# Kernel tuning notes

Measured on AMD Instinct MI355X. Metric: run time of the kernel, lower is better.

Reference implementation:

```python
import jax, jax.numpy as jnp
import numpy as np

SPARSITY_RATIO = 0.1


def setup_inputs() -> dict:
    key = jax.random.key(0)
    x = jax.random.normal(key, (4, 4096, 2048), dtype=jnp.float32)
    return {"x": x}


def reference(x):
    # x: [batch, seq_len, n_embd]
    B, S, D = x.shape
    k = max(1, int(D * SPARSITY_RATIO))
    # top-k by absolute value along the feature dim
    _, topk_idx = jax.lax.top_k(jnp.abs(x), k)  # [B, S, k]
    # scatter 1.0 at top-k positions (matches torch scatter_ mask construction)
    b = jnp.arange(B)[:, None, None]
    s = jnp.arange(S)[None, :, None]
    mask = jnp.zeros_like(x).at[b, s, topk_idx].set(1.0)
    scale = jnp.asarray(D / k, dtype=x.dtype)
    return x * mask * scale
```

## Files before the change

kernel.cpp:

```cpp
#include <hip/hip_runtime.h>


constexpr int D_DIM = 2048;
constexpr int K_SEL = 204;
constexpr int NT    = 256;
constexpr int EPL   = 32;
constexpr int RPW   = 4;

__device__ __forceinline__ int dpp_reduce_add(int x) {
    x += __builtin_amdgcn_update_dpp(0, x, 0x111, 0xF, 0xF, true);
    x += __builtin_amdgcn_update_dpp(0, x, 0x112, 0xF, 0xF, true);
    x += __builtin_amdgcn_update_dpp(0, x, 0x114, 0xF, 0xF, true);
    x += __builtin_amdgcn_update_dpp(0, x, 0x118, 0xF, 0xF, true);
    x += __builtin_amdgcn_update_dpp(0, x, 0x142, 0xA, 0xF, false);
    x += __builtin_amdgcn_update_dpp(0, x, 0x143, 0xC, 0xF, false);
    return __builtin_amdgcn_readlane(x, 63);
}

__device__ __forceinline__ int count_ge(const unsigned (&a)[EPL], unsigned t) {
    int c0 = 0, c1 = 0, c2 = 0, c3 = 0;
#pragma unroll
    for (int j = 0; j < EPL; j += 4) {
        c0 += (a[j + 0] >= t) ? 1 : 0;
        c1 += (a[j + 1] >= t) ? 1 : 0;
        c2 += (a[j + 2] >= t) ? 1 : 0;
        c3 += (a[j + 3] >= t) ? 1 : 0;
    }
    return dpp_reduce_add((c0 + c1) + (c2 + c3));
}

__device__ __forceinline__ void finish_row(const unsigned (&a)[EPL], unsigned signs,
                                           bool exact, unsigned thr, unsigned T,
                                           float* __restrict__ outr, int lane) {
    const float scale = 2048.0f / 204.0f;
    float4* op = reinterpret_cast<float4*>(outr);

    if (!exact) {
        int ge_pack = 0;
#pragma unroll
        for (int j = 0; j < EPL; ++j) {
            ge_pack += (a[j] > T) ? 1 : 0;
            ge_pack += (a[j] == T) ? (1 << 16) : 0;
        }
        const int tot = dpp_reduce_add(ge_pack);
        const int cnt_gt = tot & 0xFFFF;
        const int neq = tot >> 16;
        const int r = K_SEL - cnt_gt;

        if (neq != r) {
            const unsigned long long lt =
                (lane == 0) ? 0ull : (~0ull >> (64 - lane));
            int base = 0;
            for (int b = 0; b < 8; ++b) {
                unsigned long long m[4];
#pragma unroll
                for (int e = 0; e < 4; ++e) m[e] = __ballot(a[4 * b + e] == T);
                int cm = 0;
#pragma unroll
                for (int e = 0; e < 4; ++e) cm += __popcll(m[e] & lt);
                int partial = 0;
                float v[4];
#pragma unroll
                for (int e = 0; e < 4; ++e) {
                    const int j = 4 * b + e;
                    const int rank = base + cm + partial;
                    const bool eq = (a[j] == T);
                    const bool sel = (a[j] > T) || (eq && rank < r);
                    const float val =
                        __uint_as_float(a[j] | (((signs >> j) & 1u) << 31)) * scale;
                    v[e] = sel ? val : 0.0f;
                    partial += (int)((m[e] >> lane) & 1ull);
                }
                op[b * 64 + lane] = make_float4(v[0], v[1], v[2], v[3]);
#pragma unroll
                for (int e = 0; e < 4; ++e) base += __popcll(m[e]);
            }
            return;
        }
        thr = T;
    }

#pragma unroll
    for (int b = 0; b < 8; ++b) {
        float v[4];
#pragma unroll
        for (int e = 0; e < 4; ++e) {
            const int j = 4 * b + e;
            const float val =
                __uint_as_float(a[j] | (((signs >> j) & 1u) << 31)) * scale;
            v[e] = (a[j] >= thr) ? val : 0.0f;
        }
        op[b * 64 + lane] = make_float4(v[0], v[1], v[2], v[3]);
    }
}

__global__ __launch_bounds__(NT) void sparse_topk_kernel(const float* __restrict__ x,
                                                         float* __restrict__ out) {
    const int wave = threadIdx.x >> 6;
    const int lane = threadIdx.x & 63;
    const long long wid = (long long)blockIdx.x * 4 + wave;
    const float* base = x + wid * RPW * D_DIM;
    float* obase = out + wid * RPW * D_DIM;

    float4 nf[8];
    {
        const float4* p = reinterpret_cast<const float4*>(base);
#pragma unroll
        for (int b = 0; b < 8; ++b) nf[b] = p[b * 64 + lane];
    }

#pragma unroll 1
    for (int r = 0; r < RPW; ++r) {
        unsigned a[EPL];
        unsigned signs = 0u;
#pragma unroll
        for (int b = 0; b < 8; ++b) {
            const unsigned w0 = __float_as_uint(nf[b].x);
            const unsigned w1 = __float_as_uint(nf[b].y);
            const unsigned w2 = __float_as_uint(nf[b].z);
            const unsigned w3 = __float_as_uint(nf[b].w);
            a[4 * b + 0] = w0 & 0x7fffffffu; signs |= (w0 >> 31) << (4 * b + 0);
            a[4 * b + 1] = w1 & 0x7fffffffu; signs |= (w1 >> 31) << (4 * b + 1);
            a[4 * b + 2] = w2 & 0x7fffffffu; signs |= (w2 >> 31) << (4 * b + 2);
            a[4 * b + 3] = w3 & 0x7fffffffu; signs |= (w3 >> 31) << (4 * b + 3);
        }

        if (r + 1 < RPW) {
            const float4* pn = reinterpret_cast<const float4*>(base + (r + 1) * D_DIM);
#pragma unroll
            for (int b = 0; b < 8; ++b) nf[b] = pn[b * 64 + lane];
        }

        unsigned lo = 0u, hi = 0x7F800000u;
        unsigned thr = 0u;
        bool exact = false;
        int step = 0, lastcnt = 0;
#pragma unroll 1
        while (hi - lo > 1u) {
            unsigned mid;
            if (step == 0)      mid = 0x3FD28F5Cu;
            else if (step == 1) mid = (lastcnt > K_SEL) ? 0x3FE66666u
                                                        : 0x3FC00000u;
            else                mid = lo + ((hi - lo) >> 1);
            if (mid <= lo || mid >= hi) mid = lo + ((hi - lo) >> 1);
            ++step;
            const int cnt = count_ge(a, mid);
            lastcnt = cnt;
            if (cnt == K_SEL) { thr = mid; exact = true; break; }
            if (cnt > K_SEL) lo = mid; else hi = mid;
        }

        finish_row(a, signs, exact, thr, lo, obase + (long long)r * D_DIM, lane);
    }
}

extern "C" void kernel_launch(void* const* d_in, const int* in_sizes, int n_in,
                              void* d_out, int out_size, void* d_ws, size_t ws_size,
                              hipStream_t stream) {
    const float* x = (const float*)d_in[0];
    float* out = (float*)d_out;
    const int rows = in_sizes[0] / D_DIM;
    const int blocks = rows / (RPW * 4);
    sparse_topk_kernel<<<blocks, NT, 0, stream>>>(x, out);
}
```

Measured before the change: 242.9 us.

## Split top-k masking into threshold-search and elementwise-apply kernels

Replaces the fused per-wave kernel, which processed four rows with register prefetch, with two kernels. The first computes a per-row magnitude threshold with one row per wave, writing tie-broken rows directly and flagging them. The second re-reads the input and applies the threshold mask and scale elementwise with a grid-stride layout. This trades an extra full read of the input and a workspace round-trip for more wave-level parallelism and a bandwidth-friendly apply pass.

```diff
diff --git a/kernel.cpp b/kernel.cpp
--- a/kernel.cpp
+++ b/kernel.cpp
@@ -3,9 +3,8 @@
 
 constexpr int D_DIM = 2048;
 constexpr int K_SEL = 204;
-constexpr int NT    = 256;
 constexpr int EPL   = 32;
-constexpr int RPW   = 4;
+constexpr unsigned SKIP = 0xFFFFFFFFu;
 
 __device__ __forceinline__ int dpp_reduce_add(int x) {
     x += __builtin_amdgcn_update_dpp(0, x, 0x111, 0xF, 0xF, true);
@@ -29,128 +28,122 @@
     return dpp_reduce_add((c0 + c1) + (c2 + c3));
 }
 
-__device__ __forceinline__ void finish_row(const unsigned (&a)[EPL], unsigned signs,
-                                           bool exact, unsigned thr, unsigned T,
-                                           float* __restrict__ outr, int lane) {
-    const float scale = 2048.0f / 204.0f;
-    float4* op = reinterpret_cast<float4*>(outr);
+__global__ __launch_bounds__(256) void thresh_kernel(const float* __restrict__ x,
+                                                     float* __restrict__ out,
+                                                     unsigned* __restrict__ tbits) {
+    const int wave = threadIdx.x >> 6;
+    const int lane = threadIdx.x & 63;
+    const long long row = (long long)blockIdx.x * 4 + wave;
+    const float* xr = x + row * D_DIM;
 
-    if (!exact) {
-        int ge_pack = 0;
+    unsigned a[EPL];
+    unsigned signs = 0u;
+    const float4* xp = reinterpret_cast<const float4*>(xr);
 #pragma unroll
-        for (int j = 0; j < EPL; ++j) {
-            ge_pack += (a[j] > T) ? 1 : 0;
-            ge_pack += (a[j] == T) ? (1 << 16) : 0;
-        }
-        const int tot = dpp_reduce_add(ge_pack);
-        const int cnt_gt = tot & 0xFFFF;
-        const int neq = tot >> 16;
-        const int r = K_SEL - cnt_gt;
+    for (int b = 0; b < 8; ++b) {
+        const float4 f = xp[b * 64 + lane];
+        const unsigned w0 = __float_as_uint(f.x), w1 = __float_as_uint(f.y);
+        const unsigned w2 = __float_as_uint(f.z), w3 = __float_as_uint(f.w);
+        a[4 * b + 0] = w0 & 0x7fffffffu; signs |= (w0 >> 31) << (4 * b + 0);
+        a[4 * b + 1] = w1 & 0x7fffffffu; signs |= (w1 >> 31) << (4 * b + 1);
+        a[4 * b + 2] = w2 & 0x7fffffffu; signs |= (w2 >> 31) << (4 * b + 2);
+        a[4 * b + 3] = w3 & 0x7fffffffu; signs |= (w3 >> 31) << (4 * b + 3);
+    }
 
-        if (neq != r) {
-            const unsigned long long lt =
-                (lane == 0) ? 0ull : (~0ull >> (64 - lane));
-            int base = 0;
-            for (int b = 0; b < 8; ++b) {
-                unsigned long long m[4];
-#pragma unroll
-                for (int e = 0; e < 4; ++e) m[e] = __ballot(a[4 * b + e] == T);
-                int cm = 0;
-#pragma unroll
-                for (int e = 0; e < 4; ++e) cm += __popcll(m[e] & lt);
-                int partial = 0;
-                float v[4];
-#pragma unroll
-                for (int e = 0; e < 4; ++e) {
-                    const int j = 4 * b + e;
-                    const int rank = base + cm + partial;
-                    const bool eq = (a[j] == T);
-                    const bool sel = (a[j] > T) || (eq && rank < r);
-                    const float val =
-                        __uint_as_float(a[j] | (((signs >> j) & 1u) << 31)) * scale;
-                    v[e] = sel ? val : 0.0f;
-                    partial += (int)((m[e] >> lane) & 1ull);
-                }
-                op[b * 64 + lane] = make_float4(v[0], v[1], v[2], v[3]);
-#pragma unroll
-                for (int e = 0; e < 4; ++e) base += __popcll(m[e]);
-            }
+    unsigned lo = 0u, hi = 0x7F800000u;
+    int step = 0, lastcnt = 0;
+#pragma unroll 1
+    while (hi - lo > 1u) {
+        unsigned mid;
+        if (step == 0)      mid = 0x3FD28F5Cu;
+        else if (step == 1) mid = (lastcnt > K_SEL) ? 0x3FE66666u
+                                                    : 0x3FC00000u;
+        else                mid = lo + ((hi - lo) >> 1);
+        if (mid <= lo || mid >= hi) mid = lo + ((hi - lo) >> 1);
+        ++step;
+        const int cnt = count_ge(a, mid);
+        lastcnt = cnt;
+        if (cnt == K_SEL) {
+            if (lane == 0) tbits[row] = mid;
             return;
         }
-        thr = T;
+        if (cnt > K_SEL) lo = mid; else hi = mid;
     }
 
+    int ge_pack = 0;
 #pragma unroll
+    for (int j = 0; j < EPL; ++j) {
+        ge_pack += (a[j] > lo) ? 1 : 0;
+        ge_pack += (a[j] == lo) ? (1 << 16) : 0;
+    }
+    const int tot = dpp_reduce_add(ge_pack);
+    const int cnt_gt = tot & 0xFFFF;
+    const int neq = tot >> 16;
+    const int r = K_SEL - cnt_gt;
+
+    if (neq == r) {
+        if (lane == 0) tbits[row] = lo;
+        return;
+    }
+
+    const float scale = 2048.0f / 204.0f;
+    float4* op = reinterpret_cast<float4*>(out + row * D_DIM);
+    const unsigned long long lt = (lane == 0) ? 0ull : (~0ull >> (64 - lane));
+    int base = 0;
     for (int b = 0; b < 8; ++b) {
+        unsigned long long m[4];
+#pragma unroll
+        for (int e = 0; e < 4; ++e) m[e] = __ballot(a[4 * b + e] == lo);
+        int cm = 0;
+#pragma unroll
+        for (int e = 0; e < 4; ++e) cm += __popcll(m[e] & lt);
+        int partial = 0;
         float v[4];
 #pragma unroll
         for (int e = 0; e < 4; ++e) {
             const int j = 4 * b + e;
+            const int rank = base + cm + partial;
+            const bool sel = (a[j] > lo) || ((a[j] == lo) && rank < r);
             const float val =
                 __uint_as_float(a[j] | (((signs >> j) & 1u) << 31)) * scale;
-            v[e] = (a[j] >= thr) ? val : 0.0f;
+            v[e] = sel ? val : 0.0f;
+            partial += (int)((m[e] >> lane) & 1ull);
         }
         op[b * 64 + lane] = make_float4(v[0], v[1], v[2], v[3]);
+#pragma unroll
+        for (int e = 0; e < 4; ++e) base += __popcll(m[e]);
     }
+    if (lane == 0) tbits[row] = SKIP;
 }
 
-__global__ __launch_bounds__(NT) void sparse_topk_kernel(const float* __restrict__ x,
-                                                         float* __restrict__ out) {
-    const int wave = threadIdx.x >> 6;
-    const int lane = threadIdx.x & 63;
-    const long long wid = (long long)blockIdx.x * 4 + wave;
-    const float* base = x + wid * RPW * D_DIM;
-    float* obase = out + wid * RPW * D_DIM;
+__global__ __launch_bounds__(256) void apply_kernel(const float* __restrict__ x,
+                                                    const unsigned* __restrict__ tbits,
+                                                    float* __restrict__ out) {
+    const float scale = 2048.0f / 204.0f;
+    const int stride = gridDim.x * blockDim.x;
+    const int i0 = blockIdx.x * blockDim.x + threadIdx.x;
+    const float4* xp = reinterpret_cast<const float4*>(x);
+    float4* op = reinterpret_cast<float4*>(out);
 
-    float4 nf[8];
-    {
-        const float4* p = reinterpret_cast<const float4*>(base);
+    int idx[4];
+    float4 f[4];
+    unsigned tb[4];
 #pragma unroll
-        for (int b = 0; b < 8; ++b) nf[b] = p[b * 64 + lane];
-    }
+    for (int q = 0; q < 4; ++q) idx[q] = i0 + q * stride;
+#pragma unroll
+    for (int q = 0; q < 4; ++q) f[q] = xp[idx[q]];
+#pragma unroll
+    for (int q = 0; q < 4; ++q) tb[q] = tbits[idx[q] >> 9];
 
-#pragma unroll 1
-    for (int r = 0; r < RPW; ++r) {
-        unsigned a[EPL];
-        unsigned signs = 0u;
 #pragma unroll
-        for (int b = 0; b < 8; ++b) {
-            const unsigned w0 = __float_as_uint(nf[b].x);
-            const unsigned w1 = __float_as_uint(nf[b].y);
-            const unsigned w2 = __float_as_uint(nf[b].z);
-            const unsigned w3 = __float_as_uint(nf[b].w);
-            a[4 * b + 0] = w0 & 0x7fffffffu; signs |= (w0 >> 31) << (4 * b + 0);
-            a[4 * b + 1] = w1 & 0x7fffffffu; signs |= (w1 >> 31) << (4 * b + 1);
-            a[4 * b + 2] = w2 & 0x7fffffffu; signs |= (w2 >> 31) << (4 * b + 2);
-            a[4 * b + 3] = w3 & 0x7fffffffu; signs |= (w3 >> 31) << (4 * b + 3);
-        }
-
-        if (r + 1 < RPW) {
-            const float4* pn = reinterpret_cast<const float4*>(base + (r + 1) * D_DIM);
-#pragma unroll
-            for (int b = 0; b < 8; ++b) nf[b] = pn[b * 64 + lane];
-        }
-
-        unsigned lo = 0u, hi = 0x7F800000u;
-        unsigned thr = 0u;
-        bool exact = false;
-        int step = 0, lastcnt = 0;
-#pragma unroll 1
-        while (hi - lo > 1u) {
-            unsigned mid;
-            if (step == 0)      mid = 0x3FD28F5Cu;
-            else if (step == 1) mid = (lastcnt > K_SEL) ? 0x3FE66666u
-                                                        : 0x3FC00000u;
-            else                mid = lo + ((hi - lo) >> 1);
-            if (mid <= lo || mid >= hi) mid = lo + ((hi - lo) >> 1);
-            ++step;
-            const int cnt = count_ge(a, mid);
-            lastcnt = cnt;
-            if (cnt == K_SEL) { thr = mid; exact = true; break; }
-            if (cnt > K_SEL) lo = mid; else hi = mid;
-        }
-
-        finish_row(a, signs, exact, thr, lo, obase + (long long)r * D_DIM, lane);
+    for (int q = 0; q < 4; ++q) {
+        if (tb[q] == SKIP) continue;
+        float4 g;
+        g.x = ((__float_as_uint(f[q].x) & 0x7fffffffu) >= tb[q]) ? f[q].x * scale : 0.0f;
+        g.y = ((__float_as_uint(f[q].y) & 0x7fffffffu) >= tb[q]) ? f[q].y * scale : 0.0f;
+        g.z = ((__float_as_uint(f[q].z) & 0x7fffffffu) >= tb[q]) ? f[q].z * scale : 0.0f;
+        g.w = ((__float_as_uint(f[q].w) & 0x7fffffffu) >= tb[q]) ? f[q].w * scale : 0.0f;
+        op[idx[q]] = g;
     }
 }
 
@@ -159,7 +152,12 @@
                               hipStream_t stream) {
     const float* x = (const float*)d_in[0];
     float* out = (float*)d_out;
+    unsigned* tbits = (unsigned*)d_ws;
     const int rows = in_sizes[0] / D_DIM;
-    const int blocks = rows / (RPW * 4);
-    sparse_topk_kernel<<<blocks, NT, 0, stream>>>(x, out);
+
+    thresh_kernel<<<rows / 4, 256, 0, stream>>>(x, out, tbits);
+
+    const int n4 = in_sizes[0] / 4;
+    const int blocks = n4 / (256 * 4);
+    apply_kernel<<<blocks, 256, 0, stream>>>(x, tbits, out);
 }
```

Measured after the change: 247.8 us. 1.02x slower.
